# Kernel optimization log

Hardware: AMD Instinct MI355X
Metric: run time of the kernel (lower is better)

The kernel has to match this reference:

```python
import jax, jax.numpy as jnp
import numpy as np

N = 20000
E = 320000
BS = 1
FG = FN = FE = 128
H = 256


def _mlp_params(key, din, dout):
    dims = [(din, H), (H, H), (H, H), (H, dout)]
    ks = jax.random.split(key, 8)
    ws = [jax.random.normal(ks[2 * i], (a, b), jnp.float32) * (1.0 / np.sqrt(a).astype(np.float32)) for i, (a, b) in enumerate(dims)]
    bs = [jax.random.normal(ks[2 * i + 1], (b,), jnp.float32) * 0.01 for i, (a, b) in enumerate(dims)]
    return ws, bs


def setup_inputs() -> dict:
    key = jax.random.key(0)
    kg, kn, ke, ks, kr, kpe, kpn, kpg = jax.random.split(key, 8)
    inp = {
        'g': jax.random.normal(kg, (BS, FG), jnp.float32),
        'nodes': jax.random.normal(kn, (BS, N, FN), jnp.float32),
        'edges': jax.random.normal(ke, (BS, E, FE), jnp.float32),
        'senders': jax.random.randint(ks, (E,), 0, N, dtype=jnp.int32),
        'receivers': jax.random.randint(kr, (E,), 0, N, dtype=jnp.int32),
    }
    for prefix, kk, din, dout in [('e', kpe, FG + 2 * FN + FE, FE), ('n', kpn, FG + FN + FE, FN), ('g', kpg, FG + FN + FE, FG)]:
        ws, bs = _mlp_params(kk, din, dout)
        for i in range(4):
            inp[f'{prefix}w{i + 1}'] = ws[i]
            inp[f'{prefix}b{i + 1}'] = bs[i]
    return inp


def _mlp(x, w1, b1, w2, b2, w3, b3, w4, b4):
    h = jax.nn.relu(x @ w1 + b1)
    h = jax.nn.relu(h @ w2 + b2)
    h = jax.nn.relu(h @ w3 + b3)
    return h @ w4 + b4


def reference(g, nodes, edges, senders, receivers,
              ew1, eb1, ew2, eb2, ew3, eb3, ew4, eb4,
              nw1, nb1, nw2, nb2, nw3, nb3, nw4, nb4,
              gw1, gb1, gw2, gb2, gw3, gb3, gw4, gb4):
    bs, n_nodes, _ = nodes.shape
    n_edges = edges.shape[1]
    # edge update: concat(g, n_sender, n_receiver, e) -> 4-layer MLP
    g_e = jnp.broadcast_to(g[:, None, :], (bs, n_edges, g.shape[-1]))
    ns = nodes[:, senders]   # [bs, E, FN] gather
    nr = nodes[:, receivers]
    e_new = _mlp(jnp.concatenate([g_e, ns, nr, edges], axis=-1), ew1, eb1, ew2, eb2, ew3, eb3, ew4, eb4)
    # node update: sum of incoming (receiver-indexed) edge feats, scatter-add
    agg = jax.vmap(lambda e: jax.ops.segment_sum(e, receivers, num_segments=n_nodes))(e_new)  # [bs, N, FE]
    g_n = jnp.broadcast_to(g[:, None, :], (bs, n_nodes, g.shape[-1]))
    n_new = _mlp(jnp.concatenate([g_n, nodes, agg], axis=-1), nw1, nb1, nw2, nb2, nw3, nb3, nw4, nb4)
    # graph update: global sums of updated edge and node feats
    e_sum = e_new.sum(axis=1)  # [bs, FE]
    n_sum = n_new.sum(axis=1)  # [bs, FN]
    g_new = _mlp(jnp.concatenate([g, n_sum, e_sum], axis=-1), gw1, gb1, gw2, gb2, gw3, gb3, gw4, gb4)
    return e_new, n_new, g_new
```

## Files before the change

kernel.cpp:

```cpp
#include <hip/hip_runtime.h>
#include <stdint.h>

typedef __attribute__((ext_vector_type(8))) short bf16x8;
typedef __attribute__((ext_vector_type(4))) float f32x4;

#define NE 320000
#define NNODES 20000
#define SMEM_BYTES 69632

__device__ __forceinline__ unsigned short f2bf(float f) {
  union { float f; unsigned int u; } v; v.f = f;
  unsigned int u = v.u;
  u += 0x7fffu + ((u >> 16) & 1u);
  return (unsigned short)(u >> 16);
}

__device__ __forceinline__ void gload_lds16(const void* g, void* l) {
  __builtin_amdgcn_global_load_lds((const __attribute__((address_space(1))) void*)g,
                                   (__attribute__((address_space(3))) void*)l, 16, 0, 0);
}

struct PackArgs {
  const float* src[8];
  unsigned short* dst[8];
  int K[8];
  int N[8];
};

__global__ void pack_weights(PackArgs a) {
  int m = blockIdx.y;
  int K = a.K[m], N = a.N[m];
  int NG = N >> 4;
  int total = (K >> 5) * NG * 64;
  int idx = blockIdx.x * 256 + threadIdx.x;
  if (idx >= total) return;
  int ln = idx & 63, f = idx >> 6;
  int g = f % NG, s = f / NG;
  const float* src = a.src[m];
  int krow = s * 32 + ((ln >> 4) & 3) * 8;
  int col = g * 16 + (ln & 15);
  bf16x8 p;
#pragma unroll
  for (int j = 0; j < 8; ++j) p[j] = (short)f2bf(src[(size_t)(krow + j) * N + col]);
  *(bf16x8*)(a.dst[m] + (size_t)idx * 8) = p;
}

__device__ __forceinline__ bf16x8 cvt8(const f32x4& a, const f32x4& b) {
  bf16x8 r;
#pragma unroll
  for (int j = 0; j < 4; ++j) {
    r[j] = (short)f2bf(a[j]);
    r[4 + j] = (short)f2bf(b[j]);
  }
  return r;
}

__device__ __forceinline__ void store_H(char* Hb, const float* biasL, int boff,
                                        f32x4 (&acc)[2][4], int wm, int wn, int t, int cl) {
#pragma unroll
  for (int mg = 0; mg < 2; ++mg) {
    int m = wm * 32 + mg * 16 + cl;
    int sw = (m & 7) << 4;
    int mb = m * 512;
#pragma unroll
    for (int g = 0; g < 4; ++g) {
      int n = wn * 64 + g * 16 + t * 4;
      f32x4 bv = *(const f32x4*)(biasL + boff + n);
      f32x4 v = acc[mg][g] + bv;
#pragma unroll
      for (int j = 0; j < 4; ++j) v[j] = fmaxf(v[j], 0.0f);
      unsigned lo = (unsigned)f2bf(v[0]) | ((unsigned)f2bf(v[1]) << 16);
      unsigned hi = (unsigned)f2bf(v[2]) | ((unsigned)f2bf(v[3]) << 16);
      *(unsigned*)(Hb + ((mb + n * 2) ^ sw)) = lo;
      *(unsigned*)(Hb + ((mb + n * 2 + 4) ^ sw)) = hi;
      f32x4 z = {0.f, 0.f, 0.f, 0.f};
      acc[mg][g] = z;
    }
  }
}

template <int MODE>
__global__ __launch_bounds__(512, 4) void fused_mlp(
    const float* __restrict__ gvec, const float* __restrict__ nodes,
    const float* __restrict__ third, const int* __restrict__ senders,
    const int* __restrict__ receivers, const unsigned short* __restrict__ pwAll,
    const float* __restrict__ b1, const float* __restrict__ b2,
    const float* __restrict__ b3, const float* __restrict__ b4,
    float* __restrict__ outp, float* __restrict__ aggp, float* __restrict__ colsum) {
  constexpr int K1 = (MODE == 0) ? 512 : 384;
  constexpr int C1 = K1 / 32;
  constexpr int CT = C1 + 8 + 8 + 4;
  constexpr int NROWS = (MODE == 0) ? NE : NNODES;

  extern __shared__ char smem[];
  char* Hb = smem;
  char* Wb0 = smem + 32768;
  char* Wb1 = smem + 49152;
  float* biasL = (float*)(smem + 65536);
  float* csL = (float*)(smem + 69120);

  const int tid = threadIdx.x;
  const int lane = tid & 63;
  const int wv = tid >> 6;
  const int wn = wv & 3;
  const int wm = wv >> 2;
  const int t = lane >> 4, cl = lane & 15;
  const int row0 = blockIdx.x * 64;

  for (int i = tid; i < 896; i += 512) {
    float bvv;
    if (i < 256) bvv = b1[i];
    else if (i < 512) bvv = b2[i - 256];
    else if (i < 768) bvv = b3[i - 512];
    else bvv = b4[i - 768];
    biasL[i] = bvv;
  }
  if (tid < 128) csL[tid] = 0.0f;

  int ri[2], r1[2], r2[2];
#pragma unroll
  for (int mg = 0; mg < 2; ++mg) {
    int i = row0 + wm * 32 + mg * 16 + cl;
    if (MODE == 0) {
      ri[mg] = i;
      r1[mg] = senders[i];
      r2[mg] = receivers[i];
    } else {
      int iv = i < NROWS ? i : (NROWS - 1);
      ri[mg] = iv;
      r1[mg] = iv;
      r2[mg] = iv;
    }
  }

  auto stageW = [&](int gc) {
    if (gc >= CT) return;
    const char* p = (const char*)pwAll + (size_t)gc * 16384;
    char* d = (gc & 1) ? Wb1 : Wb0;
    const int s0 = wv << 1;
    gload_lds16(p + (s0 << 10) + lane * 16, d + (s0 << 10));
    gload_lds16(p + ((s0 + 1) << 10) + lane * 16, d + ((s0 + 1) << 10));
  };

  f32x4 xfA[2][2], xfB[2][2];
#define LOAD_X(BUF, c)                                                              \
  {                                                                                 \
    _Pragma("unroll") for (int mg = 0; mg < 2; ++mg) {                              \
      const int k0 = (c) * 32;                                                      \
      const int reg = k0 >> 7;                                                      \
      const int off = (k0 & 127) + t * 8;                                           \
      const float* sp;                                                              \
      if (MODE == 0) {                                                              \
        sp = (reg == 0)   ? gvec + off                                              \
             : (reg == 1) ? nodes + (size_t)r1[mg] * 128 + off                      \
             : (reg == 2) ? nodes + (size_t)r2[mg] * 128 + off                      \
                          : third + (size_t)ri[mg] * 128 + off;                     \
      } else {                                                                      \
        sp = (reg == 0)   ? gvec + off                                              \
             : (reg == 1) ? nodes + (size_t)r1[mg] * 128 + off                      \
                          : third + (size_t)r2[mg] * 128 + off;                     \
      }                                                                             \
      BUF[mg][0] = *(const f32x4*)sp;                                               \
      BUF[mg][1] = *(const f32x4*)(sp + 4);                                         \
    }                                                                               \
  }

#define L1_STEP(XFC, XFN, c)                                                        \
  {                                                                                 \
    __syncthreads();                                                                \
    stageW((c) + 1);                                                                \
    if ((c) + 1 < C1) LOAD_X(XFN, (c) + 1);                                         \
    bf16x8 xb[2];                                                                   \
    _Pragma("unroll") for (int mg = 0; mg < 2; ++mg)                                \
        xb[mg] = cvt8(XFC[mg][0], XFC[mg][1]);                                      \
    const char* wb = ((c) & 1) ? Wb1 : Wb0;                                         \
    _Pragma("unroll") for (int g = 0; g < 4; ++g) {                                 \
      bf16x8 af = *(const bf16x8*)(wb + ((wn * 4 + g) << 10) + lane * 16);          \
      _Pragma("unroll") for (int mg = 0; mg < 2; ++mg)                              \
          acc[mg][g] =                                                              \
              __builtin_amdgcn_mfma_f32_16x16x32_bf16(af, xb[mg], acc[mg][g], 0, 0, 0); \
    }                                                                               \
  }

  f32x4 acc[2][4];
  {
    f32x4 z = {0.f, 0.f, 0.f, 0.f};
#pragma unroll
    for (int mg = 0; mg < 2; ++mg)
#pragma unroll
      for (int g = 0; g < 4; ++g) acc[mg][g] = z;
  }

  stageW(0);
  LOAD_X(xfA, 0);

#pragma unroll
  for (int cc = 0; cc < C1 / 2; ++cc) {
    L1_STEP(xfA, xfB, 2 * cc);
    L1_STEP(xfB, xfA, 2 * cc + 1);
  }
  store_H(Hb, biasL, 0, acc, wm, wn, t, cl);

#pragma unroll
  for (int L = 0; L < 2; ++L) {
    const int base = C1 + L * 8;
#pragma unroll
    for (int c = 0; c < 8; ++c) {
      __syncthreads();
      stageW(base + c + 1);
      const char* wb = ((base + c) & 1) ? Wb1 : Wb0;
      bf16x8 bfm[2];
#pragma unroll
      for (int mg = 0; mg < 2; ++mg) {
        int m = wm * 32 + mg * 16 + cl;
        int off = (m * 512 + c * 64 + t * 16) ^ ((m & 7) << 4);
        bfm[mg] = *(const bf16x8*)(Hb + off);
      }
#pragma unroll
      for (int g = 0; g < 4; ++g) {
        bf16x8 af = *(const bf16x8*)(wb + ((wn * 4 + g) << 10) + lane * 16);
#pragma unroll
        for (int mg = 0; mg < 2; ++mg)
          acc[mg][g] = __builtin_amdgcn_mfma_f32_16x16x32_bf16(af, bfm[mg], acc[mg][g], 0, 0, 0);
      }
    }
    __syncthreads();
    store_H(Hb, biasL, 256 + L * 256, acc, wm, wn, t, cl);
  }

  {
    const int base = C1 + 16;
#pragma unroll
    for (int c = 0; c < 4; ++c) {
      __syncthreads();
      stageW(base + c + 1);
      const char* wb = ((base + c) & 1) ? Wb1 : Wb0;
#pragma unroll
      for (int s2 = 0; s2 < 2; ++s2) {
        bf16x8 bfm[2];
#pragma unroll
        for (int mg = 0; mg < 2; ++mg) {
          int m = wm * 32 + mg * 16 + cl;
          int off = (m * 512 + c * 128 + s2 * 64 + t * 16) ^ ((m & 7) << 4);
          bfm[mg] = *(const bf16x8*)(Hb + off);
        }
#pragma unroll
        for (int g = 0; g < 2; ++g) {
          bf16x8 af = *(const bf16x8*)(wb + ((s2 * 8 + wn * 2 + g) << 10) + lane * 16);
#pragma unroll
          for (int mg = 0; mg < 2; ++mg)
            acc[mg][g] = __builtin_amdgcn_mfma_f32_16x16x32_bf16(af, bfm[mg], acc[mg][g], 0, 0, 0);
        }
      }
    }
  }
  __syncthreads();

#pragma unroll
  for (int mg = 0; mg < 2; ++mg) {
    int m = wm * 32 + mg * 16 + cl;
    int sw = (m & 7) << 4;
    int mb = m * 512;
#pragma unroll
    for (int g = 0; g < 2; ++g) {
      int n = wn * 32 + g * 16 + t * 4;
      f32x4 bv = *(const f32x4*)(biasL + 768 + n);
      f32x4 v = acc[mg][g] + bv;
      float2 p0 = {v[0], v[1]}, p1 = {v[2], v[3]};
      *(float2*)(Hb + ((mb + n * 4) ^ sw)) = p0;
      *(float2*)(Hb + ((mb + n * 4 + 8) ^ sw)) = p1;
    }
  }
  __syncthreads();

  {
    float cs[2] = {0.f, 0.f};
#pragma unroll
    for (int rr = 0; rr < 8; ++rr) {
      int r = wv * 8 + rr;
      int e = row0 + r;
      bool valid = (MODE == 0) ? true : (e < NROWS);
      int rcv = (MODE == 0 && valid) ? receivers[e] : 0;
      float vh[2];
#pragma unroll
      for (int h = 0; h < 2; ++h) {
        int off = (r * 512 + (h * 64 + lane) * 4) ^ ((r & 7) << 4);
        float v = *(const float*)(Hb + off);
        vh[h] = valid ? v : 0.0f;
      }
      if (valid) {
        float* op = outp + (size_t)e * 128 + lane;
        op[0] = vh[0];
        op[64] = vh[1];
        if (MODE == 0) {
          float* ap = aggp + (size_t)rcv * 128 + lane;
          atomicAdd(ap, vh[0]);
          atomicAdd(ap + 64, vh[1]);
        }
      }
      cs[0] += vh[0];
      cs[1] += vh[1];
    }
    atomicAdd(&csL[lane], cs[0]);
    atomicAdd(&csL[64 + lane], cs[1]);
  }
  __syncthreads();
  if (tid < 128) atomicAdd(colsum + tid, csL[tid]);
#undef LOAD_X
#undef L1_STEP
}

__global__ void global_mlp(const float* __restrict__ g, const float* __restrict__ nsum,
                           const float* __restrict__ esum, const float* __restrict__ w1,
                           const float* __restrict__ bb1, const float* __restrict__ w2,
                           const float* __restrict__ bb2, const float* __restrict__ w3,
                           const float* __restrict__ bb3, const float* __restrict__ w4,
                           const float* __restrict__ bb4, float* __restrict__ outg) {
  __shared__ float x[384], h1[256], h2[256], h3[256];
  int tq = threadIdx.x;
  if (tq < 128) x[tq] = g[tq];
  else if (tq < 256) x[tq] = nsum[tq - 128];
  else x[tq] = esum[tq - 256];
  __syncthreads();
  if (tq < 256) {
    float a = bb1[tq];
    for (int k = 0; k < 384; ++k) a = fmaf(x[k], w1[k * 256 + tq], a);
    h1[tq] = fmaxf(a, 0.f);
  }
  __syncthreads();
  if (tq < 256) {
    float a = bb2[tq];
    for (int k = 0; k < 256; ++k) a = fmaf(h1[k], w2[k * 256 + tq], a);
    h2[tq] = fmaxf(a, 0.f);
  }
  __syncthreads();
  if (tq < 256) {
    float a = bb3[tq];
    for (int k = 0; k < 256; ++k) a = fmaf(h2[k], w3[k * 256 + tq], a);
    h3[tq] = fmaxf(a, 0.f);
  }
  __syncthreads();
  if (tq < 128) {
    float a = bb4[tq];
    for (int k = 0; k < 256; ++k) a = fmaf(h3[k], w4[k * 128 + tq], a);
    outg[tq] = a;
  }
}

extern "C" void kernel_launch(void* const* d_in, const int* in_sizes, int n_in, void* d_out,
                              int out_size, void* d_ws, size_t ws_size, hipStream_t stream) {
  const float* g = (const float*)d_in[0];
  const float* nodes = (const float*)d_in[1];
  const float* edges = (const float*)d_in[2];
  const int* senders = (const int*)d_in[3];
  const int* receivers = (const int*)d_in[4];
  const float* ew[4] = {(const float*)d_in[5], (const float*)d_in[7], (const float*)d_in[9],
                        (const float*)d_in[11]};
  const float* eb[4] = {(const float*)d_in[6], (const float*)d_in[8], (const float*)d_in[10],
                        (const float*)d_in[12]};
  const float* nw[4] = {(const float*)d_in[13], (const float*)d_in[15], (const float*)d_in[17],
                        (const float*)d_in[19]};
  const float* nb[4] = {(const float*)d_in[14], (const float*)d_in[16], (const float*)d_in[18],
                        (const float*)d_in[20]};
  const float* gw[4] = {(const float*)d_in[21], (const float*)d_in[23], (const float*)d_in[25],
                        (const float*)d_in[27]};
  const float* gb[4] = {(const float*)d_in[22], (const float*)d_in[24], (const float*)d_in[26],
                        (const float*)d_in[28]};

  float* out = (float*)d_out;
  float* e_new = out;
  float* n_new = out + (size_t)NE * 128;
  float* g_new = n_new + (size_t)NNODES * 128;

  char* ws = (char*)d_ws;
  unsigned short* pe1 = (unsigned short*)ws;
  unsigned short* pe2 = pe1 + 512 * 256;
  unsigned short* pe3 = pe2 + 256 * 256;
  unsigned short* pe4 = pe3 + 256 * 256;
  unsigned short* pn1 = pe4 + 256 * 128;
  unsigned short* pn2 = pn1 + 384 * 256;
  unsigned short* pn3 = pn2 + 256 * 256;
  unsigned short* pn4 = pn3 + 256 * 256;
  float* agg = (float*)(ws + 1114112);
  float* esum = agg + (size_t)NNODES * 128;
  float* nsum = esum + 128;

  hipMemsetAsync(agg, 0, (size_t)NNODES * 128 * 4 + 1024, stream);

  PackArgs pa;
  const float* srcs[8] = {ew[0], ew[1], ew[2], ew[3], nw[0], nw[1], nw[2], nw[3]};
  unsigned short* dsts[8] = {pe1, pe2, pe3, pe4, pn1, pn2, pn3, pn4};
  int Ks[8] = {512, 256, 256, 256, 384, 256, 256, 256};
  int Ns[8] = {256, 256, 256, 128, 256, 256, 256, 128};
  for (int i = 0; i < 8; ++i) {
    pa.src[i] = srcs[i];
    pa.dst[i] = dsts[i];
    pa.K[i] = Ks[i];
    pa.N[i] = Ns[i];
  }
  pack_weights<<<dim3(64, 8), 256, 0, stream>>>(pa);

  hipFuncSetAttribute((const void*)&fused_mlp<0>, hipFuncAttributeMaxDynamicSharedMemorySize,
                      SMEM_BYTES);
  hipFuncSetAttribute((const void*)&fused_mlp<1>, hipFuncAttributeMaxDynamicSharedMemorySize,
                      SMEM_BYTES);

  fused_mlp<0><<<NE / 64, 512, SMEM_BYTES, stream>>>(
      g, nodes, edges, senders, receivers, pe1, eb[0], eb[1], eb[2], eb[3], e_new, agg, esum);
  fused_mlp<1><<<(NNODES + 63) / 64, 512, SMEM_BYTES, stream>>>(
      g, nodes, agg, senders, receivers, pn1, nb[0], nb[1], nb[2], nb[3], n_new, nullptr, nsum);
  global_mlp<<<1, 384, 0, stream>>>(g, nsum, esum, gw[0], gb[0], gw[1], gb[1], gw[2], gb[2], gw[3],
                                    gb[3], g_new);
}
```

Measured before the change: 560.1 us.

## Replace atomic scatter-add aggregation with CSR-sorted gather-based segment sum

```diff
diff --git a/kernel.cpp b/kernel.cpp
--- a/kernel.cpp
+++ b/kernel.cpp
@@ -45,6 +45,74 @@
   *(bf16x8*)(a.dst[m] + (size_t)idx * 8) = p;
 }
 
+__global__ void hist_recv(const int* __restrict__ receivers, int* __restrict__ counts) {
+  int e = blockIdx.x * 256 + threadIdx.x;
+  if (e < NE) atomicAdd(&counts[receivers[e]], 1);
+}
+
+__global__ void scan_offsets(const int* __restrict__ counts, int* __restrict__ offsets,
+                             int* __restrict__ cursor) {
+  __shared__ int tsum[1024];
+  int t = threadIdx.x;
+  int loc[20];
+  int s = 0;
+  if (t < 1000) {
+    int base = t * 20;
+#pragma unroll
+    for (int j = 0; j < 20; ++j) {
+      loc[j] = counts[base + j];
+      s += loc[j];
+    }
+  }
+  tsum[t] = s;
+  __syncthreads();
+  for (int d = 1; d < 1024; d <<= 1) {
+    int v = (t >= d) ? tsum[t - d] : 0;
+    __syncthreads();
+    tsum[t] += v;
+    __syncthreads();
+  }
+  if (t < 1000) {
+    int run = (t == 0) ? 0 : tsum[t - 1];
+    int base = t * 20;
+#pragma unroll
+    for (int j = 0; j < 20; ++j) {
+      offsets[base + j] = run;
+      cursor[base + j] = run;
+      run += loc[j];
+    }
+  }
+  if (t == 0) offsets[NNODES] = tsum[1023];
+}
+
+__global__ void scatter_eidx(const int* __restrict__ receivers, int* __restrict__ cursor,
+                             int* __restrict__ eidx) {
+  int e = blockIdx.x * 256 + threadIdx.x;
+  if (e >= NE) return;
+  int pos = atomicAdd(&cursor[receivers[e]], 1);
+  eidx[pos] = e;
+}
+
+__global__ __launch_bounds__(256) void aggregate(const int* __restrict__ offsets,
+                                                 const int* __restrict__ eidx,
+                                                 const float* __restrict__ e_new,
+                                                 float* __restrict__ agg) {
+  int n = blockIdx.x * 2 + (threadIdx.x >> 7);
+  if (n >= NNODES) return;
+  int col = threadIdx.x & 127;
+  int j = offsets[n], jend = offsets[n + 1];
+  float s0 = 0.f, s1 = 0.f, s2 = 0.f, s3 = 0.f;
+  for (; j + 3 < jend; j += 4) {
+    int e0 = eidx[j], e1 = eidx[j + 1], e2 = eidx[j + 2], e3 = eidx[j + 3];
+    s0 += e_new[(size_t)e0 * 128 + col];
+    s1 += e_new[(size_t)e1 * 128 + col];
+    s2 += e_new[(size_t)e2 * 128 + col];
+    s3 += e_new[(size_t)e3 * 128 + col];
+  }
+  for (; j < jend; ++j) s0 += e_new[(size_t)eidx[j] * 128 + col];
+  agg[(size_t)n * 128 + col] = (s0 + s1) + (s2 + s3);
+}
+
 __device__ __forceinline__ bf16x8 cvt8(const f32x4& a, const f32x4& b) {
   bf16x8 r;
 #pragma unroll
@@ -86,7 +154,7 @@
     const int* __restrict__ receivers, const unsigned short* __restrict__ pwAll,
     const float* __restrict__ b1, const float* __restrict__ b2,
     const float* __restrict__ b3, const float* __restrict__ b4,
-    float* __restrict__ outp, float* __restrict__ aggp, float* __restrict__ colsum) {
+    float* __restrict__ outp, float* __restrict__ colsum) {
   constexpr int K1 = (MODE == 0) ? 512 : 384;
   constexpr int C1 = K1 / 32;
   constexpr int CT = C1 + 8 + 8 + 4;
@@ -280,7 +348,6 @@
       int r = wv * 8 + rr;
       int e = row0 + r;
       bool valid = (MODE == 0) ? true : (e < NROWS);
-      int rcv = (MODE == 0 && valid) ? receivers[e] : 0;
       float vh[2];
 #pragma unroll
       for (int h = 0; h < 2; ++h) {
@@ -292,11 +359,6 @@
         float* op = outp + (size_t)e * 128 + lane;
         op[0] = vh[0];
         op[64] = vh[1];
-        if (MODE == 0) {
-          float* ap = aggp + (size_t)rcv * 128 + lane;
-          atomicAdd(ap, vh[0]);
-          atomicAdd(ap + 64, vh[1]);
-        }
       }
       cs[0] += vh[0];
       cs[1] += vh[1];
@@ -384,8 +446,13 @@
   float* agg = (float*)(ws + 1114112);
   float* esum = agg + (size_t)NNODES * 128;
   float* nsum = esum + 128;
-
-  hipMemsetAsync(agg, 0, (size_t)NNODES * 128 * 4 + 1024, stream);
+  int* counts = (int*)(nsum + 128);
+  int* offsets = counts + NNODES;
+  int* cursor = offsets + NNODES + 1;
+  int* eidx = cursor + NNODES;
+
+  hipMemsetAsync(esum, 0, 256 * 4, stream);
+  hipMemsetAsync(counts, 0, NNODES * 4, stream);
 
   PackArgs pa;
   const float* srcs[8] = {ew[0], ew[1], ew[2], ew[3], nw[0], nw[1], nw[2], nw[3]};
@@ -400,15 +467,20 @@
   }
   pack_weights<<<dim3(64, 8), 256, 0, stream>>>(pa);
 
+  hist_recv<<<(NE + 255) / 256, 256, 0, stream>>>(receivers, counts);
+  scan_offsets<<<1, 1024, 0, stream>>>(counts, offsets, cursor);
+  scatter_eidx<<<(NE + 255) / 256, 256, 0, stream>>>(receivers, cursor, eidx);
+
   hipFuncSetAttribute((const void*)&fused_mlp<0>, hipFuncAttributeMaxDynamicSharedMemorySize,
                       SMEM_BYTES);
   hipFuncSetAttribute((const void*)&fused_mlp<1>, hipFuncAttributeMaxDynamicSharedMemorySize,
                       SMEM_BYTES);
 
   fused_mlp<0><<<NE / 64, 512, SMEM_BYTES, stream>>>(
-      g, nodes, edges, senders, receivers, pe1, eb[0], eb[1], eb[2], eb[3], e_new, agg, esum);
+      g, nodes, edges, senders, receivers, pe1, eb[0], eb[1], eb[2], eb[3], e_new, esum);
+  aggregate<<<(NNODES + 1) / 2, 256, 0, stream>>>(offsets, eidx, e_new, agg);
   fused_mlp<1><<<(NNODES + 63) / 64, 512, SMEM_BYTES, stream>>>(
-      g, nodes, agg, senders, receivers, pn1, nb[0], nb[1], nb[2], nb[3], n_new, nullptr, nsum);
+      g, nodes, agg, senders, receivers, pn1, nb[0], nb[1], nb[2], nb[3], n_new, nsum);
   global_mlp<<<1, 384, 0, stream>>>(g, nsum, esum, gw[0], gb[0], gw[1], gb[1], gw[2], gb[2], gw[3],
                                     gb[3], g_new);
 }
```

New measurement: 608.3 us. 8.6% more time.
